# Kernel optimization log

Measured on AMD Instinct MI355X. Metric: run time of the kernel, lower is better.

Reference implementation:

```python
import jax, jax.numpy as jnp
import numpy as np
import math

LOG2PI = math.log(2.0 * math.pi)


def _pair_sum(m1, v1, m2, v2, w):
    """sum_{i,j} w[i,j] * exp(delta_ij) for diagonal 2-D Gaussians.

    m1,v1: [K1,2] means / diagonal variances; m2,v2: [K2,2]; w: [K1,K2].
    Closed form of the torch code's 2x2 inverse/det/mm chain exploiting the
    fact that all covariances are diagonal (cov = diag((wh/2)^2)).
    """
    ci = 1.0 / v1[:, None, :]                      # [K1,1,2] = cov_inv_i diag
    cj = 1.0 / v2[None, :, :]                      # [1,K2,2] = cov_inv_j diag
    s = ci + cj                                    # [K1,K2,2] = cov_inv_ij diag
    mij = (m1[:, None, :] * ci + m2[None, :, :] * cj) / s   # combined mean
    quad = (jnp.sum(mij * mij * s, -1)
            - jnp.sum(m1 * m1 / v1, -1)[:, None]
            - jnp.sum(m2 * m2 / v2, -1)[None, :])            # [K1,K2]
    # log(det(cov_inv_ij) / (det(cov_inv_i) * det(cov_inv_j)))
    logdet = (jnp.sum(jnp.log(s), -1)
              + jnp.sum(jnp.log(v1), -1)[:, None]
              + jnp.sum(jnp.log(v2), -1)[None, :])           # [K1,K2]
    delta = 0.5 * (quad - logdet - 2.0 * LOG2PI)   # x_dim = 2
    return jnp.sum(w * jnp.exp(delta))


def _cs_div(p_m, p_v, p_a, q_m, q_v, q_a):
    pq = _pair_sum(p_m, p_v, q_m, q_v, p_a @ q_a.T)
    pp = _pair_sum(p_m, p_v, p_m, p_v, p_a @ p_a.T)
    qq = _pair_sum(q_m, q_v, q_m, q_v, q_a @ q_a.T)
    return 2.0 * jnp.log(pq) - jnp.log(pp) - jnp.log(qq)


def _forward(pred_bboxes, pred_labels, gt_bboxes, gt_labels):
    num_classes = pred_labels.shape[2] - 1
    pred_alpha = (jax.nn.sigmoid(pred_labels[:, :, -1])[:, :, None]
                  * jax.nn.softmax(pred_labels[:, :, :-1], axis=2))   # [bs,kp,C]
    gt_alpha = jax.nn.one_hot(gt_labels, num_classes, dtype=pred_alpha.dtype)
    pred_m = pred_bboxes[:, :, :2]
    pred_v = jnp.square(pred_bboxes[:, :, 2:] / 2.0)
    gt_m = gt_bboxes[:, :, :2]
    gt_v = jnp.square(gt_bboxes[:, :, 2:] / 2.0)
    per_img = jax.vmap(_cs_div)(gt_m, gt_v, gt_alpha, pred_m, pred_v, pred_alpha)
    return -jnp.sum(per_img)


def setup_inputs() -> dict:
    key = jax.random.key(0)
    k1, k2, k3, k4 = jax.random.split(key, 4)
    BS, KP, KG, NC = 32, 1000, 100, 80
    # widths/heights must be strictly positive -> uniform in [0.05, 1)
    pred_bboxes = jax.random.uniform(k1, (BS, KP, 4), jnp.float32, 0.05, 1.0)
    pred_labels = jax.random.normal(k2, (BS, KP, NC + 1), jnp.float32)
    gt_bboxes = jax.random.uniform(k3, (BS, KG, 4), jnp.float32, 0.05, 1.0)
    gt_labels = jax.random.randint(k4, (BS, KG), 0, NC)
    return {"pred_bboxes": pred_bboxes, "pred_labels": pred_labels,
            "gt_bboxes": gt_bboxes, "gt_labels": gt_labels}


def reference(pred_bboxes, pred_labels, gt_bboxes, gt_labels):
    return _forward(pred_bboxes, pred_labels, gt_bboxes, gt_labels)
```

## Files before the change

kernel.cpp:

```cpp
#include <hip/hip_runtime.h>
#include <math.h>

#define BS 32
#define KP 1000
#define KPP 1024
#define KG 100
#define NC 80
#define SK 96
#define LP 104
#define NT 8
#define NIT 15
#define NQQ (BS * NIT)
#define NPPQ (5 * BS)
#define NALL (NQQ + NPPQ)
#define NPERIMG 20
#define GCNT 512

using bf16x8 = __attribute__((ext_vector_type(8))) short;
using f32x4  = __attribute__((ext_vector_type(4))) float;
using f32x2  = __attribute__((ext_vector_type(2))) float;

__device__ __forceinline__ float wave_reduce_sum(float v) {
#pragma unroll
    for (int m = 32; m > 0; m >>= 1) v += __shfl_xor(v, m, 64);
    return v;
}
__device__ __forceinline__ float wave_reduce_max(float v) {
#pragma unroll
    for (int m = 32; m > 0; m >>= 1) v = fmaxf(v, __shfl_xor(v, m, 64));
    return v;
}

__device__ __forceinline__ unsigned short f2bf(float f) {
    unsigned int u = __float_as_uint(f);
    u += 0x7fffu + ((u >> 16) & 1u);
    return (unsigned short)(u >> 16);
}
__device__ __forceinline__ float bf2f(unsigned short h) {
    return __uint_as_float(((unsigned int)h) << 16);
}

__device__ __forceinline__ float kval(float4 a, float4 b) {
    f32x2 S = (f32x2){a.z, a.w} + (f32x2){b.z, b.w};
    f32x2 d = (f32x2){a.x, a.y} - (f32x2){b.x, b.y};
    f32x2 d2 = d * d;
    f32x2 t = d2 * S.yx;
    float num = t.x + t.y;
    float P = S.x * S.y;
    float rs = __builtin_amdgcn_rsqf(P);
    float q = num * rs * rs;
    return 0.15915494309189535f * rs * __expf(-0.5f * q);
}

__global__ __launch_bounds__(256) void alpha_kernel(const float* __restrict__ pl,
                                                    unsigned short* __restrict__ ah,
                                                    float* __restrict__ acc) {
    if (blockIdx.x == 0) {
#pragma unroll
        for (int k = 0; k < 3; ++k) acc[threadIdx.x + 256 * k] = 0.0f;
    }
    int wave = threadIdx.x >> 6;
    int lane = threadIdx.x & 63;
    int rr = blockIdx.x * 4 + wave;
    int b = rr >> 10, r = rr & (KPP - 1);
    unsigned short* oh = ah + (size_t)rr * SK;
    if (r < KP) {
        const float* x = pl + ((size_t)b * KP + r) * (NC + 1);
        float l0 = x[lane];
        float l1 = (lane < 16) ? x[64 + lane] : -1e30f;
        float obj = x[NC];
        float m = wave_reduce_max(fmaxf(l0, l1));
        float e0 = __expf(l0 - m);
        float e1 = (lane < 16) ? __expf(l1 - m) : 0.0f;
        float s = wave_reduce_sum(e0 + e1);
        float sig = 1.0f / (1.0f + __expf(-obj));
        float sc = sig / s;
        oh[lane] = f2bf(e0 * sc);
        if (lane < 32) oh[64 + lane] = (lane < 16) ? f2bf(e1 * sc) : 0;
    } else {
        oh[lane] = 0;
        if (lane < 32) oh[64 + lane] = 0;
    }
}

__global__ __launch_bounds__(256, 3) void main_kernel(const float* __restrict__ pb,
                                                      const unsigned short* __restrict__ ahg,
                                                      const float* __restrict__ gtb,
                                                      const int* __restrict__ gtl,
                                                      float* __restrict__ acc,
                                                      float* __restrict__ out) {
    __shared__ short lds[2 * 128 * LP];
    __shared__ float red[4];
    __shared__ int last;

    int tid = threadIdx.x;
    int lane = tid & 63, w = tid >> 6;
    int bi = blockIdx.x;
    int b;

    if (bi < NQQ) {
        short* la = lds;
        short* lb = lds + 128 * LP;
        b = bi & 31;
        int p = bi >> 5;
        int it = p >> 1, half = p & 1;
        int i0 = it * 128;

        if (tid < 128) {
            int gi = i0 + tid;
            float4 v = make_float4(0.0f, 0.0f, 1.0f, 1.0f);
            if (gi < KP) {
                float4 x = ((const float4*)pb)[b * KP + gi];
                v = make_float4(x.x, x.y, 0.25f * x.z * x.z, 0.25f * x.w * x.w);
            }
            *(float4*)(la + tid * LP + 96) = v;
        }
        {
            const float4* sa = (const float4*)(ahg + ((size_t)(b << 10) + i0) * SK);
#pragma unroll
            for (int k = 0; k < 6; ++k) {
                int o = tid + k * 256;
                int row = o / 12, slot = o - row * 12;
                *(float4*)(la + row * LP + slot * 8) = sa[o];
            }
        }

        int wy = w >> 1, wx = w & 1;
        int m15 = lane & 15, quad = lane >> 4;
        int ar = wy * 64 + m15;
        int br = wx * 64 + m15;
        int jb = wx * 64 + m15;
        int ib = wy * 64 + quad * 4;

        float part = 0.0f;
        bool first = true;
        for (int jt = it + half; jt < NT; jt += 2) {
            int j0 = jt * 128;
            if (!first) __syncthreads();
            if (tid < 128) {
                int gi = j0 + tid;
                float4 v = make_float4(0.0f, 0.0f, 1.0f, 1.0f);
                if (gi < KP) {
                    float4 x = ((const float4*)pb)[b * KP + gi];
                    v = make_float4(x.x, x.y, 0.25f * x.z * x.z, 0.25f * x.w * x.w);
                }
                *(float4*)(lb + tid * LP + 96) = v;
            }
            {
                const float4* sb = (const float4*)(ahg + ((size_t)(b << 10) + j0) * SK);
#pragma unroll
                for (int k = 0; k < 6; ++k) {
                    int o = tid + k * 256;
                    int row = o / 12, slot = o - row * 12;
                    *(float4*)(lb + row * LP + slot * 8) = sb[o];
                }
            }
            __syncthreads();

            f32x4 c4[4][4];
#pragma unroll
            for (int r = 0; r < 4; ++r)
#pragma unroll
                for (int s = 0; s < 4; ++s) c4[r][s] = (f32x4){0.0f, 0.0f, 0.0f, 0.0f};

#pragma unroll
            for (int ks = 0; ks < 3; ++ks) {
                int kk = ks * 32 + quad * 8;
                bf16x8 bh[4];
#pragma unroll
                for (int cg = 0; cg < 4; ++cg)
                    bh[cg] = *(const bf16x8*)(lb + (br + cg * 16) * LP + kk);
#pragma unroll
                for (int rg = 0; rg < 4; ++rg) {
                    bf16x8 xh = *(const bf16x8*)(la + (ar + rg * 16) * LP + kk);
#pragma unroll
                    for (int cg = 0; cg < 4; ++cg)
                        c4[rg][cg] = __builtin_amdgcn_mfma_f32_16x16x32_bf16(xh, bh[cg], c4[rg][cg], 0, 0, 0);
                }
            }

            float4 pj[4];
#pragma unroll
            for (int cg = 0; cg < 4; ++cg)
                pj[cg] = *(const float4*)(lb + (jb + cg * 16) * LP + 96);
            float tpart = 0.0f;
#pragma unroll
            for (int rg = 0; rg < 4; ++rg) {
#pragma unroll
                for (int e = 0; e < 4; ++e) {
                    float4 pi = *(const float4*)(la + (ib + rg * 16 + e) * LP + 96);
#pragma unroll
                    for (int cg = 0; cg < 4; ++cg)
                        tpart += c4[rg][cg][e] * kval(pi, pj[cg]);
                }
            }
            part += (jt != it) ? 2.0f * tpart : tpart;
            first = false;
        }

        part = wave_reduce_sum(part);
        if (lane == 0) red[w] = part;
        __syncthreads();
        if (tid == 0)
            atomicAdd(&acc[b * 16 + 2], red[0] + red[1] + red[2] + red[3]);
    } else {
        int pi = bi - NQQ;
        b = pi & 31;
        int p5 = pi >> 5;
        short* lalpha = lds;
        float4* gm = (float4*)(lds + 24576);
        int* gl = (int*)(lds + 24576 + 800);
        if (tid < KG) {
            float4 x = ((const float4*)gtb)[b * KG + tid];
            gm[tid] = make_float4(x.x, x.y, 0.25f * x.z * x.z, 0.25f * x.w * x.w);
            gl[tid] = gtl[b * KG + tid];
        }
        if (p5 < 4) {
            const float4* sa = (const float4*)(ahg + ((size_t)(b << 10) + p5 * 256) * SK);
#pragma unroll
            for (int k = 0; k < 12; ++k) {
                int o = tid + k * 256;
                *(float4*)(lalpha + o * 8) = sa[o];
            }
        }
        __syncthreads();
        float part = 0.0f;
        if (p5 < 4) {
            int j = p5 * 256 + tid;
            if (j < KP) {
                float4 x = ((const float4*)pb)[b * KP + j];
                float4 pm = make_float4(x.x, x.y, 0.25f * x.z * x.z, 0.25f * x.w * x.w);
                const unsigned short* arow = (const unsigned short*)lalpha + tid * SK;
#pragma unroll 4
                for (int i = 0; i < KG; ++i) {
                    part += bf2f(arow[gl[i]]) * kval(gm[i], pm);
                }
            }
        } else {
            for (int p = tid; p < KG * KG; p += 256) {
                int i = p / KG;
                int j = p - i * KG;
                if (gl[i] == gl[j]) part += kval(gm[i], gm[j]);
            }
        }
        part = wave_reduce_sum(part);
        if (lane == 0) red[w] = part;
        __syncthreads();
        if (tid == 0) {
            float s = red[0] + red[1] + red[2] + red[3];
            atomicAdd(&acc[b * 16 + ((p5 < 4) ? 0 : 1)], s);
        }
    }

    if (tid == 0) {
        __threadfence();
        unsigned int o = atomicAdd((unsigned int*)(acc + b * 16 + 4), 1u);
        int l = 0;
        if (o == NPERIMG - 1) {
            __threadfence();
            unsigned int g = atomicAdd((unsigned int*)(acc + GCNT), 1u);
            l = (g == BS - 1) ? 1 : 0;
        }
        last = l;
    }
    __syncthreads();
    if (last && tid < 64) {
        float v = 0.0f;
        if (tid < BS) {
            float pq = atomicAdd(&acc[tid * 16 + 0], 0.0f);
            float pp = atomicAdd(&acc[tid * 16 + 1], 0.0f);
            float qq = atomicAdd(&acc[tid * 16 + 2], 0.0f);
            v = 2.0f * logf(pq) - logf(pp) - logf(qq);
        }
        v = wave_reduce_sum(v);
        if (tid == 0) out[0] = -v;
    }
}

extern "C" void kernel_launch(void* const* d_in, const int* in_sizes, int n_in,
                              void* d_out, int out_size, void* d_ws, size_t ws_size,
                              hipStream_t stream) {
    (void)in_sizes; (void)n_in; (void)out_size; (void)ws_size;
    const float* pred_bb  = (const float*)d_in[0];
    const float* pred_lab = (const float*)d_in[1];
    const float* gt_bb    = (const float*)d_in[2];
    const int*   gt_lab   = (const int*)d_in[3];
    float* out = (float*)d_out;

    unsigned short* ah = (unsigned short*)d_ws;
    float* acc = (float*)(ah + (size_t)BS * KPP * SK);

    hipLaunchKernelGGL(alpha_kernel, dim3(BS * KPP / 4), dim3(256), 0, stream,
                       pred_lab, ah, acc);
    hipLaunchKernelGGL(main_kernel, dim3(NALL), dim3(256), 0, stream,
                       pred_bb, ah, gt_bb, gt_lab, acc, out);
}
```

Baseline: 98.91 us.

## Pack bbox params into alpha rows and stage tiles via direct global-to-LDS loads

```diff
diff --git a/kernel.cpp b/kernel.cpp
--- a/kernel.cpp
+++ b/kernel.cpp
@@ -6,8 +6,9 @@
 #define KPP 1024
 #define KG 100
 #define NC 80
-#define SK 96
+#define SK 104
 #define LP 104
+#define PQS 98
 #define NT 8
 #define NIT 15
 #define NQQ (BS * NIT)
@@ -52,7 +53,24 @@
     return 0.15915494309189535f * rs * __expf(-0.5f * q);
 }
 
+__device__ __forceinline__ void stage16(short* dst, const unsigned short* src, int tid) {
+#pragma unroll
+    for (int k = 0; k < 6; ++k) {
+        int o = (tid + k * 256) * 16;
+        __builtin_amdgcn_global_load_lds(
+            (const __attribute__((address_space(1))) unsigned int*)((const char*)src + o),
+            (__attribute__((address_space(3))) unsigned int*)((char*)dst + o), 16, 0, 0);
+    }
+    if (tid < 128) {
+        int o = (1536 + tid) * 16;
+        __builtin_amdgcn_global_load_lds(
+            (const __attribute__((address_space(1))) unsigned int*)((const char*)src + o),
+            (__attribute__((address_space(3))) unsigned int*)((char*)dst + o), 16, 0, 0);
+    }
+}
+
 __global__ __launch_bounds__(256) void alpha_kernel(const float* __restrict__ pl,
+                                                    const float* __restrict__ pbb,
                                                     unsigned short* __restrict__ ah,
                                                     float* __restrict__ acc) {
     if (blockIdx.x == 0) {
@@ -77,9 +95,14 @@
         float sc = sig / s;
         oh[lane] = f2bf(e0 * sc);
         if (lane < 32) oh[64 + lane] = (lane < 16) ? f2bf(e1 * sc) : 0;
+        if (lane == 0) {
+            float4 xb = ((const float4*)pbb)[b * KP + r];
+            *(float4*)(oh + 96) = make_float4(xb.x, xb.y, 0.25f * xb.z * xb.z, 0.25f * xb.w * xb.w);
+        }
     } else {
         oh[lane] = 0;
         if (lane < 32) oh[64 + lane] = 0;
+        if (lane == 0) *(float4*)(oh + 96) = make_float4(0.0f, 0.0f, 1.0f, 1.0f);
     }
 }
 
@@ -104,26 +127,9 @@
         b = bi & 31;
         int p = bi >> 5;
         int it = p >> 1, half = p & 1;
-        int i0 = it * 128;
-
-        if (tid < 128) {
-            int gi = i0 + tid;
-            float4 v = make_float4(0.0f, 0.0f, 1.0f, 1.0f);
-            if (gi < KP) {
-                float4 x = ((const float4*)pb)[b * KP + gi];
-                v = make_float4(x.x, x.y, 0.25f * x.z * x.z, 0.25f * x.w * x.w);
-            }
-            *(float4*)(la + tid * LP + 96) = v;
-        }
-        {
-            const float4* sa = (const float4*)(ahg + ((size_t)(b << 10) + i0) * SK);
-#pragma unroll
-            for (int k = 0; k < 6; ++k) {
-                int o = tid + k * 256;
-                int row = o / 12, slot = o - row * 12;
-                *(float4*)(la + row * LP + slot * 8) = sa[o];
-            }
-        }
+        const unsigned short* abase = ahg + (size_t)(b << 10) * SK;
+
+        stage16(la, abase + (size_t)(it * 128) * SK, tid);
 
         int wy = w >> 1, wx = w & 1;
         int m15 = lane & 15, quad = lane >> 4;
@@ -135,26 +141,8 @@
         float part = 0.0f;
         bool first = true;
         for (int jt = it + half; jt < NT; jt += 2) {
-            int j0 = jt * 128;
             if (!first) __syncthreads();
-            if (tid < 128) {
-                int gi = j0 + tid;
-                float4 v = make_float4(0.0f, 0.0f, 1.0f, 1.0f);
-                if (gi < KP) {
-                    float4 x = ((const float4*)pb)[b * KP + gi];
-                    v = make_float4(x.x, x.y, 0.25f * x.z * x.z, 0.25f * x.w * x.w);
-                }
-                *(float4*)(lb + tid * LP + 96) = v;
-            }
-            {
-                const float4* sb = (const float4*)(ahg + ((size_t)(b << 10) + j0) * SK);
-#pragma unroll
-                for (int k = 0; k < 6; ++k) {
-                    int o = tid + k * 256;
-                    int row = o / 12, slot = o - row * 12;
-                    *(float4*)(lb + row * LP + slot * 8) = sb[o];
-                }
-            }
+            stage16(lb, abase + (size_t)(jt * 128) * SK, tid);
             __syncthreads();
 
             f32x4 c4[4][4];
@@ -208,8 +196,8 @@
         b = pi & 31;
         int p5 = pi >> 5;
         short* lalpha = lds;
-        float4* gm = (float4*)(lds + 24576);
-        int* gl = (int*)(lds + 24576 + 800);
+        float4* gm = (float4*)(lds + 25088);
+        int* gl = (int*)(lds + 25088 + 800);
         if (tid < KG) {
             float4 x = ((const float4*)gtb)[b * KG + tid];
             gm[tid] = make_float4(x.x, x.y, 0.25f * x.z * x.z, 0.25f * x.w * x.w);
@@ -220,7 +208,10 @@
 #pragma unroll
             for (int k = 0; k < 12; ++k) {
                 int o = tid + k * 256;
-                *(float4*)(lalpha + o * 8) = sa[o];
+                int row = o / 12, slot = o - row * 12;
+                float4 x = sa[row * 13 + slot];
+                float* dstf = (float*)(lalpha + row * PQS + slot * 8);
+                dstf[0] = x.x; dstf[1] = x.y; dstf[2] = x.z; dstf[3] = x.w;
             }
         }
         __syncthreads();
@@ -230,7 +221,7 @@
             if (j < KP) {
                 float4 x = ((const float4*)pb)[b * KP + j];
                 float4 pm = make_float4(x.x, x.y, 0.25f * x.z * x.z, 0.25f * x.w * x.w);
-                const unsigned short* arow = (const unsigned short*)lalpha + tid * SK;
+                const unsigned short* arow = (const unsigned short*)(lalpha + tid * PQS);
 #pragma unroll 4
                 for (int i = 0; i < KG; ++i) {
                     part += bf2f(arow[gl[i]]) * kval(gm[i], pm);
@@ -291,7 +282,7 @@
     float* acc = (float*)(ah + (size_t)BS * KPP * SK);
 
     hipLaunchKernelGGL(alpha_kernel, dim3(BS * KPP / 4), dim3(256), 0, stream,
-                       pred_lab, ah, acc);
+                       pred_lab, pred_bb, ah, acc);
     hipLaunchKernelGGL(main_kernel, dim3(NALL), dim3(256), 0, stream,
                        pred_bb, ah, gt_bb, gt_lab, acc, out);
 }
```

Result: no change. 97.94 us (-1.0%).
